# Performance work log

Hardware: AMD Instinct MI355X
Metric: run time of the kernel (lower is better)

Reference implementation:

```python
import jax, jax.numpy as jnp
import numpy as np
import math

D = 1024
H = 16
C = D // H
EPS = 1e-5

def layernorm(x, g, b):
    mu = jnp.mean(x, axis=-1, keepdims=True)
    var = jnp.mean(jnp.square(x - mu), axis=-1, keepdims=True)
    return (x - mu) * jax.lax.rsqrt(var + EPS) * g + b

def setup_inputs() -> dict:
    key = jax.random.key(0)
    ks = jax.random.split(key, 12)
    s = 1.0 / math.sqrt(D)
    inp = {
        "x": jax.random.normal(ks[0], (4, 2048, D), dtype=jnp.float32),
        "src_mask": jnp.ones((4, 2048), dtype=bool),
        "Wk": jax.random.normal(ks[1], (D, D), dtype=jnp.float32) * s,
        "Wq": jax.random.normal(ks[2], (D, D), dtype=jnp.float32) * s,
        "Wv": jax.random.normal(ks[3], (D, D), dtype=jnp.float32) * s,
        "Wfc": jax.random.normal(ks[4], (D, D), dtype=jnp.float32) * s,
        "bfc": jnp.zeros((D,), dtype=jnp.float32),
        "g1": jnp.ones((D,), dtype=jnp.float32),
        "b1": jnp.zeros((D,), dtype=jnp.float32),
        "g2": jnp.ones((D,), dtype=jnp.float32),
        "b2": jnp.zeros((D,), dtype=jnp.float32),
        "W1": jax.random.normal(ks[5], (D, 4 * D), dtype=jnp.float32) * s,
        "bf1": jnp.zeros((4 * D,), dtype=jnp.float32),
        "W2": jax.random.normal(ks[6], (4 * D, D), dtype=jnp.float32) * (1.0 / math.sqrt(4 * D)),
        "bf2": jnp.zeros((D,), dtype=jnp.float32),
    }
    return inp

def reference(x, src_mask, Wk, Wq, Wv, Wfc, bfc, g1, b1, g2, b2, W1, bf1, W2, bf2):
    b, s, _ = x.shape
    xl = layernorm(x, g1, b1)
    # self-attention (src_mask is unused in the original module)
    k = (xl @ Wk).reshape(b, s, H, C).transpose(0, 2, 1, 3)  # bhsc
    q = (xl @ Wq).reshape(b, s, H, C).transpose(0, 2, 1, 3)
    v = (xl @ Wv).reshape(b, s, H, C).transpose(0, 2, 1, 3)
    # NOTE: original multiplies by sqrt(c) (not divide) -- faithful quirk
    scores = jnp.einsum('bhqc,bhkc->bhqk', q, k) * math.sqrt(C)
    attn = jax.nn.softmax(scores, axis=-1)
    o = jnp.einsum('bhqk,bhkc->bhqc', attn, v)
    o = o.transpose(0, 2, 1, 3).reshape(b, s, D)
    ka = o @ Wfc + bfc
    x = ka + x
    xl2 = layernorm(x, g2, b2)
    ff = jax.nn.relu(xl2 @ W1 + bf1) @ W2 + bf2
    return ff + x
```

## Files before the change

### kernel.cpp

```cpp
#include <hip/hip_runtime.h>
#include <hip/hip_bf16.h>
#include <math.h>


typedef __hip_bfloat16 bf16_t;
typedef __bf16 bf16x8 __attribute__((ext_vector_type(8)));
typedef float f32x4 __attribute__((ext_vector_type(4)));

#define LN_EPS 1e-5f
#define QSCALE 11.541560327111707f
#define RESCALE_THR 100.0f
#define M0_PRIOR 275.0f

__device__ __forceinline__ void async_copy16(const bf16_t* g, bf16_t* l) {
  __builtin_amdgcn_global_load_lds(
      (const __attribute__((address_space(1))) void*)g,
      (__attribute__((address_space(3))) void*)l,
      16 , 0 , 0 );
}

__device__ __forceinline__ void split_bf16(float v, bf16_t& hi, bf16_t& lo) {
  hi = __float2bfloat16(v);
  lo = __float2bfloat16(v - __bfloat162float(hi));
}

template<bool SPLIT>
__global__ __launch_bounds__(256) void ln_kernel(
    const float* __restrict__ x, const float* __restrict__ g,
    const float* __restrict__ b, bf16_t* __restrict__ out_hi,
    bf16_t* __restrict__ out_lo)
{
  const int row = blockIdx.x;
  const int tid = threadIdx.x;
  const float4 v = *(const float4*)(x + (size_t)row * 1024 + tid * 4);
  float s  = v.x + v.y + v.z + v.w;
  float ss = v.x * v.x + v.y * v.y + v.z * v.z + v.w * v.w;
  for (int off = 32; off > 0; off >>= 1) {
    s  += __shfl_down(s, off);
    ss += __shfl_down(ss, off);
  }
  __shared__ float sb[4], ssb[4];
  const int wave = tid >> 6, lane = tid & 63;
  if (lane == 0) { sb[wave] = s; ssb[wave] = ss; }
  __syncthreads();
  const float tot  = sb[0] + sb[1] + sb[2] + sb[3];
  const float tots = ssb[0] + ssb[1] + ssb[2] + ssb[3];
  const float mu   = tot * (1.0f / 1024.0f);
  const float var  = tots * (1.0f / 1024.0f) - mu * mu;
  const float rstd = rsqrtf(var + LN_EPS);
  const float4 gv = *(const float4*)(g + tid * 4);
  const float4 bv = *(const float4*)(b + tid * 4);
  float y[4] = {(v.x - mu) * rstd * gv.x + bv.x,
                (v.y - mu) * rstd * gv.y + bv.y,
                (v.z - mu) * rstd * gv.z + bv.z,
                (v.w - mu) * rstd * gv.w + bv.w};
  bf16_t hi[4] __attribute__((aligned(8)));
  bf16_t lo[4] __attribute__((aligned(8)));
  #pragma unroll
  for (int i = 0; i < 4; i++) split_bf16(y[i], hi[i], lo[i]);
  uint2 ph, pl;
  __builtin_memcpy(&ph, hi, 8);
  *(uint2*)(out_hi + (size_t)row * 1024 + tid * 4) = ph;
  if (SPLIT) {
    __builtin_memcpy(&pl, lo, 8);
    *(uint2*)(out_lo + (size_t)row * 1024 + tid * 4) = pl;
  }
}

__global__ __launch_bounds__(256) void wtrans_all_kernel(
    const float* __restrict__ Wq, const float* __restrict__ Wk,
    const float* __restrict__ Wv, const float* __restrict__ Wfc,
    const float* __restrict__ W1, const float* __restrict__ W2,
    bf16_t* __restrict__ WqkH, bf16_t* __restrict__ WqkL,
    bf16_t* __restrict__ WvT, bf16_t* __restrict__ WfcT,
    bf16_t* __restrict__ W1T, bf16_t* __restrict__ W2T)
{
  const int id = blockIdx.x;
  const float* W; bf16_t* DH; bf16_t* DL = nullptr;
  int K, N, n0, k0;
  if (id < 4096) {
    K = 1024; N = 1024;
    const int local = id & 1023;
    n0 = (local & 31) * 32; k0 = (local >> 5) * 32;
    if (id < 1024)      { W = Wq;  DH = WqkH;                 DL = WqkL; }
    else if (id < 2048) { W = Wk;  DH = WqkH + 1024 * 1024;   DL = WqkL + 1024 * 1024; }
    else if (id < 3072) { W = Wv;  DH = WvT; }
    else                { W = Wfc; DH = WfcT; }
  } else if (id < 8192) {
    const int local = id - 4096;
    K = 1024; N = 4096; W = W1; DH = W1T;
    n0 = (local & 127) * 32; k0 = (local >> 7) * 32;
  } else {
    const int local = id - 8192;
    K = 4096; N = 1024; W = W2; DH = W2T;
    n0 = (local & 31) * 32; k0 = (local >> 5) * 32;
  }
  __shared__ float t[32][33];
  const int tx = threadIdx.x & 31, ty = threadIdx.x >> 5;
  #pragma unroll
  for (int r = ty; r < 32; r += 8)
    t[r][tx] = W[(size_t)(k0 + r) * N + n0 + tx];
  __syncthreads();
  #pragma unroll
  for (int r = ty; r < 32; r += 8) {
    const float v = t[tx][r];
    bf16_t hi, lo;
    split_bf16(v, hi, lo);
    DH[(size_t)(n0 + r) * K + k0 + tx] = hi;
    if (DL) DL[(size_t)(n0 + r) * K + k0 + tx] = lo;
  }
}

template<bool BIAS, bool RELU, bool RESID, bool OUTBF>
__global__ __launch_bounds__(256) void gemm_kernel(
    const bf16_t* __restrict__ A, const bf16_t* __restrict__ BT,
    const float* __restrict__ bias, const float* __restrict__ resid,
    float* __restrict__ outF, bf16_t* __restrict__ outB,
    int M, int N, int K)
{
  __shared__ __align__(16) bf16_t As[128 * 64];
  __shared__ __align__(16) bf16_t Bs[128 * 64];
  const int nblk = N >> 7;
  const int bm = blockIdx.x / nblk;
  const int bn = blockIdx.x % nblk;
  const int tid  = threadIdx.x;
  const int wave = tid >> 6;
  const int lane = tid & 63;
  const int l15  = lane & 15;
  const int quad = lane >> 4;
  const int wm = wave >> 1, wn = wave & 1;

  const int srow = lane >> 3;
  const int schunk = (lane & 7) ^ srow;
  const bf16_t* aG = A  + (size_t)(bm * 128 + wave * 32 + srow) * K + schunk * 8;
  const bf16_t* bG = BT + (size_t)(bn * 128 + wave * 32 + srow) * K + schunk * 8;

  f32x4 acc[4][4];
  #pragma unroll
  for (int i = 0; i < 4; i++)
    #pragma unroll
    for (int j = 0; j < 4; j++) acc[i][j] = (f32x4){0.f, 0.f, 0.f, 0.f};

  const int rsw = l15 & 7;

  for (int kt = 0; kt < K; kt += 64) {
    #pragma unroll
    for (int j = 0; j < 4; j++) {
      async_copy16(aG + kt + (size_t)(j * 8) * K, &As[(wave * 32 + j * 8) * 64]);
      async_copy16(bG + kt + (size_t)(j * 8) * K, &Bs[(wave * 32 + j * 8) * 64]);
    }
    __syncthreads();
    #pragma unroll
    for (int ko = 0; ko < 2; ko++) {
      bf16x8 af[4], bfr[4];
      #pragma unroll
      for (int i = 0; i < 4; i++)
        af[i]  = *(const bf16x8*)&As[(wm * 64 + i * 16 + l15) * 64 +
                                     (((ko * 4 + quad) ^ rsw) * 8)];
      #pragma unroll
      for (int j = 0; j < 4; j++)
        bfr[j] = *(const bf16x8*)&Bs[(wn * 64 + j * 16 + l15) * 64 +
                                     (((ko * 4 + quad) ^ rsw) * 8)];
      #pragma unroll
      for (int i = 0; i < 4; i++)
        #pragma unroll
        for (int j = 0; j < 4; j++)
          acc[i][j] = __builtin_amdgcn_mfma_f32_16x16x32_bf16(af[i], bfr[j], acc[i][j], 0, 0, 0);
    }
    __syncthreads();
  }

  const int gm0 = bm * 128 + wm * 64 + quad * 4;
  const int gn0 = bn * 128 + wn * 64 + l15;
  #pragma unroll
  for (int i = 0; i < 4; i++) {
    #pragma unroll
    for (int j = 0; j < 4; j++) {
      const int gn = gn0 + j * 16;
      const float bz = BIAS ? bias[gn] : 0.0f;
      #pragma unroll
      for (int r = 0; r < 4; r++) {
        const int gm = gm0 + i * 16 + r;
        float v = acc[i][j][r] + bz;
        if (RESID) v += resid[(size_t)gm * N + gn];
        if (RELU)  v = fmaxf(v, 0.0f);
        if (OUTBF) outB[(size_t)gm * N + gn] = __float2bfloat16(v);
        else       outF[(size_t)gm * N + gn] = v;
      }
    }
  }
}

__global__ __launch_bounds__(256) void gemm_split_kernel(
    const bf16_t* __restrict__ Ah, const bf16_t* __restrict__ Al,
    const bf16_t* __restrict__ Bh, const bf16_t* __restrict__ Bl,
    bf16_t* __restrict__ out_hi, bf16_t* __restrict__ out_lo,
    int M, int N, int K)
{
  __shared__ __align__(16) bf16_t AsH[128 * 32];
  __shared__ __align__(16) bf16_t AsL[128 * 32];
  __shared__ __align__(16) bf16_t BsH[128 * 32];
  __shared__ __align__(16) bf16_t BsL[128 * 32];
  const int nblk = N >> 7;
  const int bm = blockIdx.x / nblk;
  const int bn = blockIdx.x % nblk;
  const int tid  = threadIdx.x;
  const int wave = tid >> 6;
  const int lane = tid & 63;
  const int l15  = lane & 15;
  const int quad = lane >> 4;
  const int wm = wave >> 1, wn = wave & 1;

  const int srow = lane >> 2;
  const int schunk = (lane & 3) ^ ((lane >> 3) & 3);
  const size_t aOff = (size_t)(bm * 128 + wave * 32 + srow) * K + schunk * 8;
  const size_t bOff = (size_t)(bn * 128 + wave * 32 + srow) * K + schunk * 8;
  const int ldsOff0 = (wave * 32) * 32;
  const int ldsOff1 = (wave * 32 + 16) * 32;

  f32x4 acc[4][4];
  #pragma unroll
  for (int i = 0; i < 4; i++)
    #pragma unroll
    for (int j = 0; j < 4; j++) acc[i][j] = (f32x4){0.f, 0.f, 0.f, 0.f};

  const int rsw = (l15 >> 1) & 3;

  for (int kt = 0; kt < K; kt += 32) {
    async_copy16(Ah + aOff + kt, &AsH[ldsOff0]);
    async_copy16(Ah + aOff + kt + (size_t)16 * K, &AsH[ldsOff1]);
    async_copy16(Al + aOff + kt, &AsL[ldsOff0]);
    async_copy16(Al + aOff + kt + (size_t)16 * K, &AsL[ldsOff1]);
    async_copy16(Bh + bOff + kt, &BsH[ldsOff0]);
    async_copy16(Bh + bOff + kt + (size_t)16 * K, &BsH[ldsOff1]);
    async_copy16(Bl + bOff + kt, &BsL[ldsOff0]);
    async_copy16(Bl + bOff + kt + (size_t)16 * K, &BsL[ldsOff1]);
    __syncthreads();
    bf16x8 afH[4], afL[4], bfH[4], bfL[4];
    #pragma unroll
    for (int i = 0; i < 4; i++) {
      const int o = (wm * 64 + i * 16 + l15) * 32 + ((quad ^ rsw) * 8);
      afH[i] = *(const bf16x8*)&AsH[o];
      afL[i] = *(const bf16x8*)&AsL[o];
    }
    #pragma unroll
    for (int j = 0; j < 4; j++) {
      const int o = (wn * 64 + j * 16 + l15) * 32 + ((quad ^ rsw) * 8);
      bfH[j] = *(const bf16x8*)&BsH[o];
      bfL[j] = *(const bf16x8*)&BsL[o];
    }
    #pragma unroll
    for (int i = 0; i < 4; i++)
      #pragma unroll
      for (int j = 0; j < 4; j++) {
        acc[i][j] = __builtin_amdgcn_mfma_f32_16x16x32_bf16(afH[i], bfH[j], acc[i][j], 0, 0, 0);
        acc[i][j] = __builtin_amdgcn_mfma_f32_16x16x32_bf16(afH[i], bfL[j], acc[i][j], 0, 0, 0);
        acc[i][j] = __builtin_amdgcn_mfma_f32_16x16x32_bf16(afL[i], bfH[j], acc[i][j], 0, 0, 0);
      }
    __syncthreads();
  }

  const int gm0 = bm * 128 + wm * 64 + quad * 4;
  const int gn0 = bn * 128 + wn * 64 + l15;
  #pragma unroll
  for (int i = 0; i < 4; i++)
    #pragma unroll
    for (int j = 0; j < 4; j++) {
      const int gn = gn0 + j * 16;
      const float scale = (gn < 1024) ? QSCALE : 1.0f;
      #pragma unroll
      for (int r = 0; r < 4; r++) {
        const int gm = gm0 + i * 16 + r;
        bf16_t hi, lo;
        split_bf16(acc[i][j][r] * scale, hi, lo);
        out_hi[(size_t)gm * N + gn] = hi;
        out_lo[(size_t)gm * N + gn] = lo;
      }
    }
}

__global__ __launch_bounds__(256) void attn_kernel(
    const bf16_t* __restrict__ qkH,
    const bf16_t* __restrict__ qkL,
    const bf16_t* __restrict__ vT,
    bf16_t* __restrict__ o)
{
  const int qt = blockIdx.x;
  const int h  = blockIdx.y;
  const int b  = blockIdx.z;
  const int wave = threadIdx.x >> 6;
  const int lane = threadIdx.x & 63;
  const int l15  = lane & 15;
  const int quad = lane >> 4;
  const int sw   = l15 & 7;
  const int qrowA = qt * 128 + wave * 32;
  const int qrowB = qrowA + 16;

  __shared__ __align__(16) bf16_t SMEM[20480];
  bf16_t* KhL  = SMEM;
  bf16_t* KlL  = SMEM + 4096;
  bf16_t* VtL  = SMEM + 8192;
  bf16_t* pw   = SMEM + 12288 + wave * 2048;

  const size_t tok0 = (size_t)b * 2048;
  const size_t qoffA = (tok0 + qrowA + l15) * 2048 + h * 64;
  const size_t qoffB = (tok0 + qrowB + l15) * 2048 + h * 64;
  const bf16x8 aA0H = *(const bf16x8*)(qkH + qoffA + quad * 8);
  const bf16x8 aA1H = *(const bf16x8*)(qkH + qoffA + 32 + quad * 8);
  const bf16x8 aA0L = *(const bf16x8*)(qkL + qoffA + quad * 8);
  const bf16x8 aA1L = *(const bf16x8*)(qkL + qoffA + 32 + quad * 8);
  const bf16x8 aB0H = *(const bf16x8*)(qkH + qoffB + quad * 8);
  const bf16x8 aB1H = *(const bf16x8*)(qkH + qoffB + 32 + quad * 8);
  const bf16x8 aB0L = *(const bf16x8*)(qkL + qoffB + quad * 8);
  const bf16x8 aB1L = *(const bf16x8*)(qkL + qoffB + 32 + quad * 8);

  const int kOff = 1024 + h * 64;
  const int rsub = lane >> 3;
  const int csw  = (lane & 7) ^ (rsub & 7);

  f32x4 negMA = (f32x4){-M0_PRIOR, -M0_PRIOR, -M0_PRIOR, -M0_PRIOR};
  f32x4 negMB = negMA;
  f32x4 OfA[4], OfB[4];
  f32x4 lsumA = (f32x4){0.f, 0.f, 0.f, 0.f};
  f32x4 lsumB = lsumA;
  #pragma unroll
  for (int c = 0; c < 4; c++) { OfA[c] = lsumA; OfB[c] = lsumA; }

  for (int kb = 0; kb < 2048; kb += 64) {
    #pragma unroll
    for (int j = 0; j < 2; j++) {
      const int row0 = wave * 16 + j * 8;
      const size_t krow = tok0 + kb + row0 + rsub;
      async_copy16(qkH + krow * 2048 + kOff + csw * 8, &KhL[row0 * 64]);
      async_copy16(qkL + krow * 2048 + kOff + csw * 8, &KlL[row0 * 64]);
      async_copy16(vT + (size_t)(h * 64 + row0 + rsub) * 8192 + tok0 + kb + csw * 8,
                   &VtL[row0 * 64]);
    }
    __syncthreads();

    #pragma unroll
    for (int t = 0; t < 4; t++) {
      const int base = (t * 16 + l15) * 64;
      const bf16x8 bh0 = *(const bf16x8*)&KhL[base + ((quad) ^ sw) * 8];
      const bf16x8 bh1 = *(const bf16x8*)&KhL[base + ((4 + quad) ^ sw) * 8];
      const bf16x8 bl0 = *(const bf16x8*)&KlL[base + ((quad) ^ sw) * 8];
      const bf16x8 bl1 = *(const bf16x8*)&KlL[base + ((4 + quad) ^ sw) * 8];
      f32x4 accA = negMA;
      f32x4 accB = negMB;
      accA = __builtin_amdgcn_mfma_f32_16x16x32_bf16(aA0H, bh0, accA, 0, 0, 0);
      accA = __builtin_amdgcn_mfma_f32_16x16x32_bf16(aA1H, bh1, accA, 0, 0, 0);
      accA = __builtin_amdgcn_mfma_f32_16x16x32_bf16(aA0H, bl0, accA, 0, 0, 0);
      accA = __builtin_amdgcn_mfma_f32_16x16x32_bf16(aA1H, bl1, accA, 0, 0, 0);
      accA = __builtin_amdgcn_mfma_f32_16x16x32_bf16(aA0L, bh0, accA, 0, 0, 0);
      accA = __builtin_amdgcn_mfma_f32_16x16x32_bf16(aA1L, bh1, accA, 0, 0, 0);
      accB = __builtin_amdgcn_mfma_f32_16x16x32_bf16(aB0H, bh0, accB, 0, 0, 0);
      accB = __builtin_amdgcn_mfma_f32_16x16x32_bf16(aB1H, bh1, accB, 0, 0, 0);
      accB = __builtin_amdgcn_mfma_f32_16x16x32_bf16(aB0H, bl0, accB, 0, 0, 0);
      accB = __builtin_amdgcn_mfma_f32_16x16x32_bf16(aB1H, bl1, accB, 0, 0, 0);
      accB = __builtin_amdgcn_mfma_f32_16x16x32_bf16(aB0L, bh0, accB, 0, 0, 0);
      accB = __builtin_amdgcn_mfma_f32_16x16x32_bf16(aB1L, bh1, accB, 0, 0, 0);

      float pmax = fmaxf(fmaxf(fmaxf(accA[0], accA[1]), fmaxf(accA[2], accA[3])),
                         fmaxf(fmaxf(accB[0], accB[1]), fmaxf(accB[2], accB[3])));
      if (!__all(pmax <= RESCALE_THR)) {
        #pragma unroll
        for (int r = 0; r < 4; r++) {
          float mA = accA[r], mB = accB[r];
          mA = fmaxf(mA, __shfl_xor(mA, 1)); mB = fmaxf(mB, __shfl_xor(mB, 1));
          mA = fmaxf(mA, __shfl_xor(mA, 2)); mB = fmaxf(mB, __shfl_xor(mB, 2));
          mA = fmaxf(mA, __shfl_xor(mA, 4)); mB = fmaxf(mB, __shfl_xor(mB, 4));
          mA = fmaxf(mA, __shfl_xor(mA, 8)); mB = fmaxf(mB, __shfl_xor(mB, 8));
          const float sA = fmaxf(mA, 0.0f);
          const float sB = fmaxf(mB, 0.0f);
          const float fA = __builtin_amdgcn_exp2f(-sA);
          const float fB = __builtin_amdgcn_exp2f(-sB);
          negMA[r] -= sA;  negMB[r] -= sB;
          lsumA[r] *= fA;  lsumB[r] *= fB;
          #pragma unroll
          for (int c = 0; c < 4; c++) { OfA[c][r] *= fA; OfB[c][r] *= fB; }
          accA[r] -= sA;   accB[r] -= sB;
          const int RA = quad * 4 + r;
          const int RB = 16 + RA;
          #pragma unroll
          for (int tp = 0; tp < t; tp++) {
            const int iA = RA * 64 + (((tp * 2 + (l15 >> 3)) ^ (RA & 7)) * 8) + (l15 & 7);
            const int iB = RB * 64 + (((tp * 2 + (l15 >> 3)) ^ (RB & 7)) * 8) + (l15 & 7);
            pw[iA] = __float2bfloat16(__bfloat162float(pw[iA]) * fA);
            pw[iB] = __float2bfloat16(__bfloat162float(pw[iB]) * fB);
          }
        }
      }

      #pragma unroll
      for (int r = 0; r < 4; r++) {
        const float pA = __builtin_amdgcn_exp2f(accA[r]);
        const float pB = __builtin_amdgcn_exp2f(accB[r]);
        lsumA[r] += pA;
        lsumB[r] += pB;
        const int RA = quad * 4 + r;
        const int RB = 16 + RA;
        pw[RA * 64 + (((t * 2 + (l15 >> 3)) ^ (RA & 7)) * 8) + (l15 & 7)] =
            __float2bfloat16(pA);
        pw[RB * 64 + (((t * 2 + (l15 >> 3)) ^ (RB & 7)) * 8) + (l15 & 7)] =
            __float2bfloat16(pB);
      }
    }

    const bf16x8 paA0 = *(const bf16x8*)&pw[l15 * 64 + ((quad) ^ sw) * 8];
    const bf16x8 paA1 = *(const bf16x8*)&pw[l15 * 64 + ((4 + quad) ^ sw) * 8];
    const bf16x8 paB0 = *(const bf16x8*)&pw[(16 + l15) * 64 + ((quad) ^ sw) * 8];
    const bf16x8 paB1 = *(const bf16x8*)&pw[(16 + l15) * 64 + ((4 + quad) ^ sw) * 8];
    #pragma unroll
    for (int c = 0; c < 4; c++) {
      const int vb = (c * 16 + l15) * 64;
      const bf16x8 bv0 = *(const bf16x8*)&VtL[vb + ((quad) ^ sw) * 8];
      const bf16x8 bv1 = *(const bf16x8*)&VtL[vb + ((4 + quad) ^ sw) * 8];
      OfA[c] = __builtin_amdgcn_mfma_f32_16x16x32_bf16(paA0, bv0, OfA[c], 0, 0, 0);
      OfA[c] = __builtin_amdgcn_mfma_f32_16x16x32_bf16(paA1, bv1, OfA[c], 0, 0, 0);
      OfB[c] = __builtin_amdgcn_mfma_f32_16x16x32_bf16(paB0, bv0, OfB[c], 0, 0, 0);
      OfB[c] = __builtin_amdgcn_mfma_f32_16x16x32_bf16(paB1, bv1, OfB[c], 0, 0, 0);
    }
    __syncthreads();
  }

  float lrowA[4], lrowB[4];
  #pragma unroll
  for (int r = 0; r < 4; r++) {
    float cA = lsumA[r], cB = lsumB[r];
    cA += __shfl_xor(cA, 1); cB += __shfl_xor(cB, 1);
    cA += __shfl_xor(cA, 2); cB += __shfl_xor(cB, 2);
    cA += __shfl_xor(cA, 4); cB += __shfl_xor(cB, 4);
    cA += __shfl_xor(cA, 8); cB += __shfl_xor(cB, 8);
    lrowA[r] = cA; lrowB[r] = cB;
  }

  bf16_t* opA = o + (tok0 + qrowA) * 1024 + h * 64;
  bf16_t* opB = o + (tok0 + qrowB) * 1024 + h * 64;
  #pragma unroll
  for (int c = 0; c < 4; c++)
    #pragma unroll
    for (int r = 0; r < 4; r++) {
      opA[(size_t)(quad * 4 + r) * 1024 + c * 16 + l15] =
          __float2bfloat16(OfA[c][r] / lrowA[r]);
      opB[(size_t)(quad * 4 + r) * 1024 + c * 16 + l15] =
          __float2bfloat16(OfB[c][r] / lrowB[r]);
    }
}

extern "C" void kernel_launch(void* const* d_in, const int* in_sizes, int n_in,
                              void* d_out, int out_size, void* d_ws, size_t ws_size,
                              hipStream_t stream)
{
  (void)in_sizes; (void)n_in; (void)out_size; (void)ws_size;
  const float* x   = (const float*)d_in[0];
  const float* Wk  = (const float*)d_in[2];
  const float* Wq  = (const float*)d_in[3];
  const float* Wv  = (const float*)d_in[4];
  const float* Wfc = (const float*)d_in[5];
  const float* bfc = (const float*)d_in[6];
  const float* g1  = (const float*)d_in[7];
  const float* b1  = (const float*)d_in[8];
  const float* g2  = (const float*)d_in[9];
  const float* b2  = (const float*)d_in[10];
  const float* W1  = (const float*)d_in[11];
  const float* bf1 = (const float*)d_in[12];
  const float* W2  = (const float*)d_in[13];
  const float* bf2 = (const float*)d_in[14];
  float* out = (float*)d_out;

  char* ws = (char*)d_ws;
  bf16_t* xl_hi  = (bf16_t*)(ws + (0ull   << 20));
  bf16_t* oAtt   = xl_hi;
  bf16_t* xl_lo  = (bf16_t*)(ws + (16ull  << 20));
  bf16_t* vT     = xl_lo;
  bf16_t* xl2    = xl_lo;
  bf16_t* qk_hi  = (bf16_t*)(ws + (32ull  << 20));
  bf16_t* qk_lo  = (bf16_t*)(ws + (64ull  << 20));
  bf16_t* h1     = qk_hi;
  float*  x2     = (float*) (ws + (112ull << 20));
  bf16_t* Wqk_hi = (bf16_t*)(ws + (144ull << 20));
  bf16_t* Wqk_lo = (bf16_t*)(ws + (148ull << 20));
  bf16_t* WvT    = (bf16_t*)(ws + (152ull << 20));
  bf16_t* WfcT   = (bf16_t*)(ws + (154ull << 20));
  bf16_t* W1T    = (bf16_t*)(ws + (156ull << 20));
  bf16_t* W2T    = (bf16_t*)(ws + (164ull << 20));

  const dim3 blk(256);

  wtrans_all_kernel<<<12288, blk, 0, stream>>>(
      Wq, Wk, Wv, Wfc, W1, W2, Wqk_hi, Wqk_lo, WvT, WfcT, W1T, W2T);

  ln_kernel<true><<<8192, blk, 0, stream>>>(x, g1, b1, xl_hi, xl_lo);

  gemm_split_kernel<<<64 * 16, blk, 0, stream>>>(
      xl_hi, xl_lo, Wqk_hi, Wqk_lo, qk_hi, qk_lo, 8192, 2048, 1024);

  gemm_kernel<false, false, false, true><<<8 * 64, blk, 0, stream>>>(
      WvT, xl_hi, nullptr, nullptr, nullptr, vT, 1024, 8192, 1024);

  attn_kernel<<<dim3(16, 16, 4), blk, 0, stream>>>(qk_hi, qk_lo, vT, oAtt);

  gemm_kernel<true, false, true, false><<<64 * 8, blk, 0, stream>>>(
      oAtt, WfcT, bfc, x, x2, nullptr, 8192, 1024, 1024);

  ln_kernel<false><<<8192, blk, 0, stream>>>(x2, g2, b2, xl2, nullptr);

  gemm_kernel<true, true, false, true><<<64 * 32, blk, 0, stream>>>(
      xl2, W1T, bf1, nullptr, nullptr, h1, 8192, 4096, 1024);

  gemm_kernel<true, false, true, false><<<64 * 8, blk, 0, stream>>>(
      h1, W2T, bf2, x2, out, nullptr, 8192, 1024, 4096);
}
```

Baseline: 663.5 us.

## Double-buffer K tiles in LDS, load V directly to registers, split P into halves

The attention kernel now double-buffers the K hi/lo tiles in LDS, prefetching the next 64-key block while computing the current one, so there is one barrier per iteration. V is read straight from global memory into registers instead of being staged in LDS. The P tile is processed in two 32-key halves with a smaller swizzled per-wave buffer, which limits the rescale rewrite to the previous sub-tile. s_setprio hints are placed around the MFMA bursts. The risk is that global V loads are exposed to latency and that register pressure rises.

```diff
diff --git a/kernel.cpp b/kernel.cpp
--- a/kernel.cpp
+++ b/kernel.cpp
@@ -297,10 +297,7 @@
   const int qrowB = qrowA + 16;
 
   __shared__ __align__(16) bf16_t SMEM[20480];
-  bf16_t* KhL  = SMEM;
-  bf16_t* KlL  = SMEM + 4096;
-  bf16_t* VtL  = SMEM + 8192;
-  bf16_t* pw   = SMEM + 12288 + wave * 2048;
+  bf16_t* pw = SMEM + 16384 + wave * 1024;
 
   const size_t tok0 = (size_t)b * 2048;
   const size_t qoffA = (tok0 + qrowA + l15) * 2048 + h * 64;
@@ -316,7 +313,7 @@
 
   const int kOff = 1024 + h * 64;
   const int rsub = lane >> 3;
-  const int csw  = (lane & 7) ^ (rsub & 7);
+  const int csw  = (lane & 7) ^ rsub;
 
   f32x4 negMA = (f32x4){-M0_PRIOR, -M0_PRIOR, -M0_PRIOR, -M0_PRIOR};
   f32x4 negMB = negMA;
@@ -326,99 +323,120 @@
   #pragma unroll
   for (int c = 0; c < 4; c++) { OfA[c] = lsumA; OfB[c] = lsumA; }
 
-  for (int kb = 0; kb < 2048; kb += 64) {
-    #pragma unroll
-    for (int j = 0; j < 2; j++) {
-      const int row0 = wave * 16 + j * 8;
-      const size_t krow = tok0 + kb + row0 + rsub;
-      async_copy16(qkH + krow * 2048 + kOff + csw * 8, &KhL[row0 * 64]);
-      async_copy16(qkL + krow * 2048 + kOff + csw * 8, &KlL[row0 * 64]);
-      async_copy16(vT + (size_t)(h * 64 + row0 + rsub) * 8192 + tok0 + kb + csw * 8,
-                   &VtL[row0 * 64]);
-    }
-    __syncthreads();
-
-    #pragma unroll
-    for (int t = 0; t < 4; t++) {
-      const int base = (t * 16 + l15) * 64;
-      const bf16x8 bh0 = *(const bf16x8*)&KhL[base + ((quad) ^ sw) * 8];
-      const bf16x8 bh1 = *(const bf16x8*)&KhL[base + ((4 + quad) ^ sw) * 8];
-      const bf16x8 bl0 = *(const bf16x8*)&KlL[base + ((quad) ^ sw) * 8];
-      const bf16x8 bl1 = *(const bf16x8*)&KlL[base + ((4 + quad) ^ sw) * 8];
-      f32x4 accA = negMA;
-      f32x4 accB = negMB;
-      accA = __builtin_amdgcn_mfma_f32_16x16x32_bf16(aA0H, bh0, accA, 0, 0, 0);
-      accA = __builtin_amdgcn_mfma_f32_16x16x32_bf16(aA1H, bh1, accA, 0, 0, 0);
-      accA = __builtin_amdgcn_mfma_f32_16x16x32_bf16(aA0H, bl0, accA, 0, 0, 0);
-      accA = __builtin_amdgcn_mfma_f32_16x16x32_bf16(aA1H, bl1, accA, 0, 0, 0);
-      accA = __builtin_amdgcn_mfma_f32_16x16x32_bf16(aA0L, bh0, accA, 0, 0, 0);
-      accA = __builtin_amdgcn_mfma_f32_16x16x32_bf16(aA1L, bh1, accA, 0, 0, 0);
-      accB = __builtin_amdgcn_mfma_f32_16x16x32_bf16(aB0H, bh0, accB, 0, 0, 0);
-      accB = __builtin_amdgcn_mfma_f32_16x16x32_bf16(aB1H, bh1, accB, 0, 0, 0);
-      accB = __builtin_amdgcn_mfma_f32_16x16x32_bf16(aB0H, bl0, accB, 0, 0, 0);
-      accB = __builtin_amdgcn_mfma_f32_16x16x32_bf16(aB1H, bl1, accB, 0, 0, 0);
-      accB = __builtin_amdgcn_mfma_f32_16x16x32_bf16(aB0L, bh0, accB, 0, 0, 0);
-      accB = __builtin_amdgcn_mfma_f32_16x16x32_bf16(aB1L, bh1, accB, 0, 0, 0);
-
-      float pmax = fmaxf(fmaxf(fmaxf(accA[0], accA[1]), fmaxf(accA[2], accA[3])),
-                         fmaxf(fmaxf(accB[0], accB[1]), fmaxf(accB[2], accB[3])));
-      if (!__all(pmax <= RESCALE_THR)) {
+  #pragma unroll
+  for (int j = 0; j < 2; j++) {
+    const int row0 = wave * 16 + j * 8;
+    const size_t krow = tok0 + row0 + rsub;
+    async_copy16(qkH + krow * 2048 + kOff + csw * 8, &SMEM[row0 * 64]);
+    async_copy16(qkL + krow * 2048 + kOff + csw * 8, &SMEM[8192 + row0 * 64]);
+  }
+  __syncthreads();
+
+  for (int i = 0; i < 32; i++) {
+    const int kbase = i * 64;
+    const int co = (i & 1) * 4096;
+    const int no = 4096 - co;
+    if (i < 31) {
+      #pragma unroll
+      for (int j = 0; j < 2; j++) {
+        const int row0 = wave * 16 + j * 8;
+        const size_t krow = tok0 + kbase + 64 + row0 + rsub;
+        async_copy16(qkH + krow * 2048 + kOff + csw * 8, &SMEM[no + row0 * 64]);
+        async_copy16(qkL + krow * 2048 + kOff + csw * 8, &SMEM[8192 + no + row0 * 64]);
+      }
+    }
+    const bf16_t* KhC = SMEM + co;
+    const bf16_t* KlC = SMEM + 8192 + co;
+
+    #pragma unroll
+    for (int half = 0; half < 2; half++) {
+      bf16x8 bv[4];
+      #pragma unroll
+      for (int c = 0; c < 4; c++)
+        bv[c] = *(const bf16x8*)(vT + (size_t)(h * 64 + c * 16 + l15) * 8192 +
+                                 tok0 + kbase + half * 32 + quad * 8);
+
+      #pragma unroll
+      for (int tl = 0; tl < 2; tl++) {
+        const int t = half * 2 + tl;
+        const int base = (t * 16 + l15) * 64;
+        const bf16x8 bh0 = *(const bf16x8*)&KhC[base + ((quad) ^ sw) * 8];
+        const bf16x8 bh1 = *(const bf16x8*)&KhC[base + ((4 + quad) ^ sw) * 8];
+        const bf16x8 bl0 = *(const bf16x8*)&KlC[base + ((quad) ^ sw) * 8];
+        const bf16x8 bl1 = *(const bf16x8*)&KlC[base + ((4 + quad) ^ sw) * 8];
+        f32x4 accA = negMA;
+        f32x4 accB = negMB;
+        __builtin_amdgcn_s_setprio(1);
+        accA = __builtin_amdgcn_mfma_f32_16x16x32_bf16(aA0H, bh0, accA, 0, 0, 0);
+        accA = __builtin_amdgcn_mfma_f32_16x16x32_bf16(aA1H, bh1, accA, 0, 0, 0);
+        accA = __builtin_amdgcn_mfma_f32_16x16x32_bf16(aA0H, bl0, accA, 0, 0, 0);
+        accA = __builtin_amdgcn_mfma_f32_16x16x32_bf16(aA1H, bl1, accA, 0, 0, 0);
+        accA = __builtin_amdgcn_mfma_f32_16x16x32_bf16(aA0L, bh0, accA, 0, 0, 0);
+        accA = __builtin_amdgcn_mfma_f32_16x16x32_bf16(aA1L, bh1, accA, 0, 0, 0);
+        accB = __builtin_amdgcn_mfma_f32_16x16x32_bf16(aB0H, bh0, accB, 0, 0, 0);
+        accB = __builtin_amdgcn_mfma_f32_16x16x32_bf16(aB1H, bh1, accB, 0, 0, 0);
+        accB = __builtin_amdgcn_mfma_f32_16x16x32_bf16(aB0H, bl0, accB, 0, 0, 0);
+        accB = __builtin_amdgcn_mfma_f32_16x16x32_bf16(aB1H, bl1, accB, 0, 0, 0);
+        accB = __builtin_amdgcn_mfma_f32_16x16x32_bf16(aB0L, bh0, accB, 0, 0, 0);
+        accB = __builtin_amdgcn_mfma_f32_16x16x32_bf16(aB1L, bh1, accB, 0, 0, 0);
+        __builtin_amdgcn_s_setprio(0);
+
+        float pmax = fmaxf(fmaxf(fmaxf(accA[0], accA[1]), fmaxf(accA[2], accA[3])),
+                           fmaxf(fmaxf(accB[0], accB[1]), fmaxf(accB[2], accB[3])));
+        if (!__all(pmax <= RESCALE_THR)) {
+          #pragma unroll
+          for (int r = 0; r < 4; r++) {
+            float mA = accA[r], mB = accB[r];
+            mA = fmaxf(mA, __shfl_xor(mA, 1)); mB = fmaxf(mB, __shfl_xor(mB, 1));
+            mA = fmaxf(mA, __shfl_xor(mA, 2)); mB = fmaxf(mB, __shfl_xor(mB, 2));
+            mA = fmaxf(mA, __shfl_xor(mA, 4)); mB = fmaxf(mB, __shfl_xor(mB, 4));
+            mA = fmaxf(mA, __shfl_xor(mA, 8)); mB = fmaxf(mB, __shfl_xor(mB, 8));
+            const float sA = fmaxf(mA, 0.0f);
+            const float sB = fmaxf(mB, 0.0f);
+            const float fA = __builtin_amdgcn_exp2f(-sA);
+            const float fB = __builtin_amdgcn_exp2f(-sB);
+            negMA[r] -= sA;  negMB[r] -= sB;
+            lsumA[r] *= fA;  lsumB[r] *= fB;
+            #pragma unroll
+            for (int c = 0; c < 4; c++) { OfA[c][r] *= fA; OfB[c][r] *= fB; }
+            accA[r] -= sA;   accB[r] -= sB;
+            if (tl == 1) {
+              const int RA = quad * 4 + r;
+              const int RB = 16 + RA;
+              const int ksw = (RA >> 1) & 3;
+              const int iA = RA * 32 + (((l15 >> 3) ^ ksw) * 8) + (l15 & 7);
+              const int iB = RB * 32 + (((l15 >> 3) ^ ksw) * 8) + (l15 & 7);
+              pw[iA] = __float2bfloat16(__bfloat162float(pw[iA]) * fA);
+              pw[iB] = __float2bfloat16(__bfloat162float(pw[iB]) * fB);
+            }
+          }
+        }
+
         #pragma unroll
         for (int r = 0; r < 4; r++) {
-          float mA = accA[r], mB = accB[r];
-          mA = fmaxf(mA, __shfl_xor(mA, 1)); mB = fmaxf(mB, __shfl_xor(mB, 1));
-          mA = fmaxf(mA, __shfl_xor(mA, 2)); mB = fmaxf(mB, __shfl_xor(mB, 2));
-          mA = fmaxf(mA, __shfl_xor(mA, 4)); mB = fmaxf(mB, __shfl_xor(mB, 4));
-          mA = fmaxf(mA, __shfl_xor(mA, 8)); mB = fmaxf(mB, __shfl_xor(mB, 8));
-          const float sA = fmaxf(mA, 0.0f);
-          const float sB = fmaxf(mB, 0.0f);
-          const float fA = __builtin_amdgcn_exp2f(-sA);
-          const float fB = __builtin_amdgcn_exp2f(-sB);
-          negMA[r] -= sA;  negMB[r] -= sB;
-          lsumA[r] *= fA;  lsumB[r] *= fB;
-          #pragma unroll
-          for (int c = 0; c < 4; c++) { OfA[c][r] *= fA; OfB[c][r] *= fB; }
-          accA[r] -= sA;   accB[r] -= sB;
+          const float pA = __builtin_amdgcn_exp2f(accA[r]);
+          const float pB = __builtin_amdgcn_exp2f(accB[r]);
+          lsumA[r] += pA;
+          lsumB[r] += pB;
           const int RA = quad * 4 + r;
           const int RB = 16 + RA;
-          #pragma unroll
-          for (int tp = 0; tp < t; tp++) {
-            const int iA = RA * 64 + (((tp * 2 + (l15 >> 3)) ^ (RA & 7)) * 8) + (l15 & 7);
-            const int iB = RB * 64 + (((tp * 2 + (l15 >> 3)) ^ (RB & 7)) * 8) + (l15 & 7);
-            pw[iA] = __float2bfloat16(__bfloat162float(pw[iA]) * fA);
-            pw[iB] = __float2bfloat16(__bfloat162float(pw[iB]) * fB);
-          }
+          const int chunk = tl * 2 + (l15 >> 3);
+          const int ksw = (RA >> 1) & 3;
+          pw[RA * 32 + ((chunk ^ ksw) * 8) + (l15 & 7)] = __float2bfloat16(pA);
+          pw[RB * 32 + ((chunk ^ ksw) * 8) + (l15 & 7)] = __float2bfloat16(pB);
         }
       }
 
-      #pragma unroll
-      for (int r = 0; r < 4; r++) {
-        const float pA = __builtin_amdgcn_exp2f(accA[r]);
-        const float pB = __builtin_amdgcn_exp2f(accB[r]);
-        lsumA[r] += pA;
-        lsumB[r] += pB;
-        const int RA = quad * 4 + r;
-        const int RB = 16 + RA;
-        pw[RA * 64 + (((t * 2 + (l15 >> 3)) ^ (RA & 7)) * 8) + (l15 & 7)] =
-            __float2bfloat16(pA);
-        pw[RB * 64 + (((t * 2 + (l15 >> 3)) ^ (RB & 7)) * 8) + (l15 & 7)] =
-            __float2bfloat16(pB);
+      const int psw = (l15 >> 1) & 3;
+      const bf16x8 paA = *(const bf16x8*)&pw[l15 * 32 + ((quad ^ psw) * 8)];
+      const bf16x8 paB = *(const bf16x8*)&pw[(16 + l15) * 32 + ((quad ^ psw) * 8)];
+      __builtin_amdgcn_s_setprio(1);
+      #pragma unroll
+      for (int c = 0; c < 4; c++) {
+        OfA[c] = __builtin_amdgcn_mfma_f32_16x16x32_bf16(paA, bv[c], OfA[c], 0, 0, 0);
+        OfB[c] = __builtin_amdgcn_mfma_f32_16x16x32_bf16(paB, bv[c], OfB[c], 0, 0, 0);
       }
-    }
-
-    const bf16x8 paA0 = *(const bf16x8*)&pw[l15 * 64 + ((quad) ^ sw) * 8];
-    const bf16x8 paA1 = *(const bf16x8*)&pw[l15 * 64 + ((4 + quad) ^ sw) * 8];
-    const bf16x8 paB0 = *(const bf16x8*)&pw[(16 + l15) * 64 + ((quad) ^ sw) * 8];
-    const bf16x8 paB1 = *(const bf16x8*)&pw[(16 + l15) * 64 + ((4 + quad) ^ sw) * 8];
-    #pragma unroll
-    for (int c = 0; c < 4; c++) {
-      const int vb = (c * 16 + l15) * 64;
-      const bf16x8 bv0 = *(const bf16x8*)&VtL[vb + ((quad) ^ sw) * 8];
-      const bf16x8 bv1 = *(const bf16x8*)&VtL[vb + ((4 + quad) ^ sw) * 8];
-      OfA[c] = __builtin_amdgcn_mfma_f32_16x16x32_bf16(paA0, bv0, OfA[c], 0, 0, 0);
-      OfA[c] = __builtin_amdgcn_mfma_f32_16x16x32_bf16(paA1, bv1, OfA[c], 0, 0, 0);
-      OfB[c] = __builtin_amdgcn_mfma_f32_16x16x32_bf16(paB0, bv0, OfB[c], 0, 0, 0);
-      OfB[c] = __builtin_amdgcn_mfma_f32_16x16x32_bf16(paB1, bv1, OfB[c], 0, 0, 0);
+      __builtin_amdgcn_s_setprio(0);
     }
     __syncthreads();
   }
```

Result: no change. 674.2 us (+1.6%).
